# Kernel tuning notes

Measured on AMD Instinct MI355X. Metric: run time of the kernel, lower is better.

Reference implementation:

```python
import jax, jax.numpy as jnp
import numpy as np

NH = 4
TEMP = 0.5

def _ln(x, w, b):
    mu = x.mean(-1, keepdims=True)
    var = ((x - mu) ** 2).mean(-1, keepdims=True)
    return (x - mu) / jnp.sqrt(var + 1e-5) * w + b

def _encoder(x, bias, key_pad, layers):
    # pre-LN torch TransformerEncoder, relu FFN, dropout=0
    Wqkv, bqkv, Wo, bo, ln1w, ln1b, ln2w, ln2b, W1, b1, W2, b2 = layers
    B, L, H = x.shape
    d = H // NH
    scale = 1.0 / np.sqrt(d)
    for i in range(Wqkv.shape[0]):
        y = _ln(x, ln1w[i], ln1b[i])
        qkv = y @ Wqkv[i].T + bqkv[i]
        q, k, v = jnp.split(qkv, 3, axis=-1)
        q = q.reshape(B, L, NH, d).transpose(0, 2, 1, 3)
        k = k.reshape(B, L, NH, d).transpose(0, 2, 1, 3)
        v = v.reshape(B, L, NH, d).transpose(0, 2, 1, 3)
        s = jnp.einsum('bhqd,bhkd->bhqk', q, k) * scale
        if bias is not None:
            s = s + bias
        s = s + key_pad[:, None, None, :]
        a = jax.nn.softmax(s, axis=-1)
        o = jnp.einsum('bhqk,bhkd->bhqd', a, v).transpose(0, 2, 1, 3).reshape(B, L, H)
        x = x + o @ Wo[i].T + bo[i]
        y = _ln(x, ln2w[i], ln2b[i])
        x = x + jax.nn.relu(y @ W1[i].T + b1[i]) @ W2[i].T + b2[i]
    return x

def _layer_params(key, nl, H, F, sc=0.05):
    ks = jax.random.split(key, 4)
    return (jax.random.normal(ks[0], (nl, 3 * H, H)) * sc, jnp.zeros((nl, 3 * H)),
            jax.random.normal(ks[1], (nl, H, H)) * sc, jnp.zeros((nl, H)),
            jnp.ones((nl, H)), jnp.zeros((nl, H)), jnp.ones((nl, H)), jnp.zeros((nl, H)),
            jax.random.normal(ks[2], (nl, F, H)) * sc, jnp.zeros((nl, F)),
            jax.random.normal(ks[3], (nl, H, F)) * sc, jnp.zeros((nl, H)))

def setup_inputs():
    key = jax.random.key(0)
    IN, H, ED, F = 64, 128, 16, 256
    G, NPG = 8, 512
    N = G * NPG
    m, k = 4, 16
    T = N
    S = T * m
    EPS = 24
    E_loc = S * EPS
    E = 65536
    ks = jax.random.split(key, 13)
    x = jax.random.normal(ks[0], (N, IN))
    log_probs = -jnp.abs(jax.random.normal(ks[1], (S,)))
    root = jnp.repeat(jnp.arange(T), m)
    base = (root // NPG) * NPG
    rest = base[:, None] + jax.random.randint(ks[2], (S, k - 1), 0, NPG)
    nodes_sampled = jnp.concatenate([root[:, None], rest], axis=1)
    valid = jnp.ones((S * k,), dtype=bool)
    edge_index_sampled = jax.random.randint(ks[3], (2, E_loc), 0, k)
    edge_ptr = jnp.arange(S + 1) * EPS
    ea_flat = jax.random.normal(ks[4], (E_loc, ED))
    src = jax.random.randint(ks[5], (E,), 0, N)
    dst = (src // NPG) * NPG + jax.random.randint(ks[6], (E,), 0, NPG)
    edge_index = jnp.stack([src, dst])
    edge_attr = jax.random.normal(ks[7], (E, ED))
    batch_vec = jnp.arange(N) // NPG
    ptr = jnp.arange(G + 1) * NPG
    d = dict(x=x, log_probs=log_probs, ea_flat=ea_flat, edge_attr=edge_attr,
             init_W=jax.random.normal(ks[8], (H, IN + 2)) * 0.05, init_b=jnp.zeros((H,)),
             loc_ep_W=jax.random.normal(ks[9], (NH, ED)) * 0.05, loc_ep_b=jnp.zeros((NH,)),
             glob_ep_W=jax.random.normal(ks[10], (NH, ED)) * 0.05, glob_ep_b=jnp.zeros((NH,)),
             loc_nw=jnp.ones((H,)), loc_nb=jnp.zeros((H,)),
             glob_nw=jnp.ones((H,)), glob_nb=jnp.zeros((H,)),
             nodes_sampled=nodes_sampled, edge_index_sampled=edge_index_sampled,
             edge_ptr=edge_ptr, edge_index=edge_index, batch_vec=batch_vec,
             ptr=ptr, valid=valid)
    names = ['Wqkv', 'bqkv', 'Wo', 'bo', 'ln1w', 'ln1b', 'ln2w', 'ln2b', 'W1', 'b1', 'W2', 'b2']
    for n, a in zip(names, _layer_params(ks[11], 4, H, F)):
        d['loc_' + n] = a
    for n, a in zip(names, _layer_params(ks[12], 4, H, F)):
        d['glob_' + n] = a
    return d

def reference(x, log_probs, ea_flat, edge_attr, init_W, init_b, loc_ep_W, loc_ep_b,
              glob_ep_W, glob_ep_b, loc_nw, loc_nb, glob_nw, glob_nb,
              loc_Wqkv, loc_bqkv, loc_Wo, loc_bo, loc_ln1w, loc_ln1b, loc_ln2w, loc_ln2b,
              loc_W1, loc_b1, loc_W2, loc_b2,
              glob_Wqkv, glob_bqkv, glob_Wo, glob_bo, glob_ln1w, glob_ln1b, glob_ln2w, glob_ln2b,
              glob_W1, glob_b1, glob_W2, glob_b2,
              nodes_sampled, edge_index_sampled, edge_ptr, edge_index, batch_vec, ptr, valid):
    S, k = nodes_sampled.shape
    N = x.shape[0]
    T = N
    m = S // T
    G = ptr.shape[0] - 1
    max_N = N // G  # equal-size graphs
    H = init_W.shape[0]
    # ---- phase 1: flatten subgraphs + init features ----
    x_flat = x[nodes_sampled.reshape(-1)]                         # [S*k, IN]
    root_global = jnp.repeat(jnp.arange(T), m)                    # [S]
    root_local = jnp.argmax(nodes_sampled == root_global[:, None], axis=1)
    root_mask = jnp.zeros((S * k,), x.dtype).at[jnp.arange(S) * k + root_local].set(1.0)
    lp = jnp.where(jnp.isfinite(log_probs), log_probs, 0.0)
    lp_flat = jnp.repeat(lp, k)[:, None] * valid[:, None].astype(x.dtype)
    h = jnp.concatenate([x_flat, lp_flat, root_mask[:, None]], axis=1) @ init_W.T + init_b
    # ---- local edge bias (scatter-add) ----
    E_loc = ea_flat.shape[0]
    sub = jnp.searchsorted(edge_ptr, jnp.arange(E_loc), side='right') - 1
    eap = ea_flat @ loc_ep_W.T + loc_ep_b                         # [E_loc, NH]
    lbias = jnp.zeros((S, k, k, NH), x.dtype).at[sub, edge_index_sampled[0], edge_index_sampled[1]].add(eap).transpose(0, 3, 1, 2)
    v2 = valid.reshape(S, k)
    key_pad_l = jnp.where(v2, 0.0, -1e9).astype(x.dtype)
    loc_layers = (loc_Wqkv, loc_bqkv, loc_Wo, loc_bo, loc_ln1w, loc_ln1b, loc_ln2w, loc_ln2b, loc_W1, loc_b1, loc_W2, loc_b2)
    out = _encoder(h.reshape(S, k, H), lbias, key_pad_l, loc_layers)
    out = _ln(out, loc_nw, loc_nb)
    vf = v2.astype(x.dtype)[..., None]
    sub_embs = (out * vf).sum(1) / jnp.maximum(vf.sum(1), 1.0)    # [S, H]
    # ---- weighted-mean aggregation over m samples per target node ----
    w = jax.nn.softmax(log_probs.reshape(T, m) / TEMP, axis=1)
    node_embs = jnp.einsum('tm,tmh->th', w, sub_embs.reshape(T, m, H))
    # ---- global phase: to_dense_batch + edge-bias transformer ----
    pos = jnp.arange(N) - ptr[batch_vec]
    dense = jnp.zeros((G, max_N, H), x.dtype).at[batch_vec, pos].set(node_embs)
    vmask = jnp.zeros((G, max_N), bool).at[batch_vec, pos].set(True)
    g = batch_vec[edge_index[0]]
    sl = edge_index[0] - ptr[g]
    dl = edge_index[1] - ptr[g]
    eag = edge_attr @ glob_ep_W.T + glob_ep_b
    gbias = jnp.zeros((G, max_N, max_N, NH), x.dtype).at[g, sl, dl].add(eag).transpose(0, 3, 1, 2)
    key_pad_g = jnp.where(vmask, 0.0, -1e9).astype(x.dtype)
    glob_layers = (glob_Wqkv, glob_bqkv, glob_Wo, glob_bo, glob_ln1w, glob_ln1b, glob_ln2w, glob_ln2b, glob_W1, glob_b1, glob_W2, glob_b2)
    gout = _encoder(dense, gbias, key_pad_g, glob_layers)
    gout = _ln(gout, glob_nw, glob_nb)
    return (gout * vmask[..., None].astype(x.dtype)).sum(1)      # [G, H]
```

## Files before the change

### kernel.cpp

```cpp
#include <hip/hip_runtime.h>
#include <math.h>

#define IN_F      64
#define H_DIM     128
#define NH_       4
#define DH_       32
#define FF_DIM    256
#define KSUB      16
#define S_SEQ     16384
#define E_LOC     393216
#define G_NUM     8
#define NPG_      512
#define N_NODES   4096
#define E_GLOB    65536
#define NLAYERS   4
#define SCALE_ATT 0.17677669529663687f

#define WQKV_SZ   (3*H_DIM*H_DIM)
#define WO_SZ     (H_DIM*H_DIM)
#define W1_SZ     (FF_DIM*H_DIM)
#define W2_SZ     (H_DIM*FF_DIM)

#define ATT(sg)   (4352 + (sg) * 2560)
#define PS_OFF    9472
#define STG_SZ    10112

typedef __bf16 bf16x8 __attribute__((ext_vector_type(8)));
typedef float  f32x4  __attribute__((ext_vector_type(4)));

__device__ __forceinline__ unsigned short f2bf(float f) {
    unsigned u = __float_as_uint(f);
    unsigned r = (u + 0x7fffu + ((u >> 16) & 1u)) >> 16;
    return (unsigned short)r;
}

__device__ __forceinline__ unsigned cvt_pk(float lo, float hi) {
    unsigned r;
    asm("v_cvt_pk_bf16_f32 %0, %1, %2" : "=v"(r) : "v"(lo), "v"(hi));
    return r;
}

__device__ __forceinline__ f32x4 mfma16(bf16x8 a, bf16x8 b, f32x4 c) {
    return __builtin_amdgcn_mfma_f32_16x16x32_bf16(a, b, c, 0, 0, 0);
}

__device__ __forceinline__ void ln_to_row(const float (&X)[8][4],
    const float* __restrict__ w, const float* __restrict__ b,
    unsigned short* rowb, int r, int q)
{
    float s1[4] = {0,0,0,0}, s2[4] = {0,0,0,0};
    #pragma unroll
    for (int t = 0; t < 8; ++t)
        #pragma unroll
        for (int i = 0; i < 4; ++i) { float v = X[t][i]; s1[i] += v; s2[i] += v*v; }
    #pragma unroll
    for (int i = 0; i < 4; ++i) {
        float a = s1[i], c = s2[i];
        a += __shfl_xor(a, 1, 16); a += __shfl_xor(a, 2, 16);
        a += __shfl_xor(a, 4, 16); a += __shfl_xor(a, 8, 16);
        c += __shfl_xor(c, 1, 16); c += __shfl_xor(c, 2, 16);
        c += __shfl_xor(c, 4, 16); c += __shfl_xor(c, 8, 16);
        float mu = a * (1.f / H_DIM);
        float var = c * (1.f / H_DIM) - mu * mu;
        s1[i] = mu; s2[i] = rsqrtf(fmaxf(var, 0.f) + 1e-5f);
    }
    for (int t = 0; t < 8; ++t) {
        float wv = w[t * 16 + r], bv = b[t * 16 + r];
        float v0 = (X[t][0] - s1[0]) * s2[0] * wv + bv;
        float v1 = (X[t][1] - s1[1]) * s2[1] * wv + bv;
        float v2 = (X[t][2] - s1[2]) * s2[2] * wv + bv;
        float v3 = (X[t][3] - s1[3]) * s2[3] * wv + bv;
        unsigned lo = cvt_pk(v0, v1), hi = cvt_pk(v2, v3);
        rowb[(q * 4 + 0) * 136 + t * 16 + r] = (unsigned short)lo;
        rowb[(q * 4 + 1) * 136 + t * 16 + r] = (unsigned short)(lo >> 16);
        rowb[(q * 4 + 2) * 136 + t * 16 + r] = (unsigned short)hi;
        rowb[(q * 4 + 3) * 136 + t * 16 + r] = (unsigned short)(hi >> 16);
    }
}

__device__ __forceinline__ void ln_mean_out(const float (&X)[8][4],
    const float* __restrict__ fnw, const float* __restrict__ fnb,
    float* __restrict__ dst, int r, int q)
{
    float s1[4] = {0,0,0,0}, s2[4] = {0,0,0,0};
    #pragma unroll
    for (int t = 0; t < 8; ++t)
        #pragma unroll
        for (int i = 0; i < 4; ++i) { float v = X[t][i]; s1[i] += v; s2[i] += v*v; }
    #pragma unroll
    for (int i = 0; i < 4; ++i) {
        float a = s1[i], c = s2[i];
        a += __shfl_xor(a, 1, 16); a += __shfl_xor(a, 2, 16);
        a += __shfl_xor(a, 4, 16); a += __shfl_xor(a, 8, 16);
        c += __shfl_xor(c, 1, 16); c += __shfl_xor(c, 2, 16);
        c += __shfl_xor(c, 4, 16); c += __shfl_xor(c, 8, 16);
        float mu = a * (1.f / H_DIM);
        float var = c * (1.f / H_DIM) - mu * mu;
        s1[i] = mu; s2[i] = rsqrtf(fmaxf(var, 0.f) + 1e-5f);
    }
    float colsum[8];
    #pragma unroll
    for (int t = 0; t < 8; ++t) {
        float wv = fnw[t * 16 + r], bv = fnb[t * 16 + r];
        float cs = 0.f;
        #pragma unroll
        for (int i = 0; i < 4; ++i) cs += (X[t][i] - s1[i]) * s2[i] * wv + bv;
        cs += __shfl_xor(cs, 16, 64);
        cs += __shfl_xor(cs, 32, 64);
        colsum[t] = cs;
    }
    float c0 = (q == 0) ? colsum[0] : (q == 1) ? colsum[1] : (q == 2) ? colsum[2] : colsum[3];
    float c1 = (q == 0) ? colsum[4] : (q == 1) ? colsum[5] : (q == 2) ? colsum[6] : colsum[7];
    dst[q * 16 + r]       = c0 * (1.f / KSUB);
    dst[(q + 4) * 16 + r] = c1 * (1.f / KSUB);
}

__global__ __launch_bounds__(256) void conv_all_k(
    const float* __restrict__ lWqkv, const float* __restrict__ lWo,
    const float* __restrict__ lW1, const float* __restrict__ lW2,
    const float* __restrict__ x,
    const float* __restrict__ gWqkv, const float* __restrict__ gWo,
    const float* __restrict__ gW1, const float* __restrict__ gW2,
    const float* __restrict__ init_W,
    unsigned short* __restrict__ wq_b, unsigned short* __restrict__ wo_b,
    unsigned short* __restrict__ w1_b, unsigned short* __restrict__ w2_b,
    unsigned short* __restrict__ x_b,
    unsigned short* __restrict__ gwq_b, unsigned short* __restrict__ gwo_b,
    unsigned short* __restrict__ gw1_b, unsigned short* __restrict__ gw2_b,
    unsigned short* __restrict__ wi_b)
{
    int b = blockIdx.x, t = threadIdx.x;
    const float* src; unsigned short* dst; int base;
    if (b < 768)       { src = lWqkv; dst = wq_b;  base = b; }
    else if (b < 1024) { src = lWo;   dst = wo_b;  base = b - 768; }
    else if (b < 1536) { src = lW1;   dst = w1_b;  base = b - 1024; }
    else if (b < 2048) { src = lW2;   dst = w2_b;  base = b - 1536; }
    else if (b < 3072) { src = x;     dst = x_b;   base = b - 2048; }
    else if (b < 3840) { src = gWqkv; dst = gwq_b; base = b - 3072; }
    else if (b < 4096) { src = gWo;   dst = gwo_b; base = b - 3840; }
    else if (b < 4608) { src = gW1;   dst = gw1_b; base = b - 4096; }
    else if (b < 5120) { src = gW2;   dst = gw2_b; base = b - 4608; }
    else {
        int i = (b - 5120) * 256 + t;
        int row = i >> 6, c = i & 63;
        wi_b[i] = f2bf(init_W[row * 66 + c]);
        return;
    }
    int i = base * 256 + t;
    dst[i] = f2bf(src[i]);
}

__global__ __launch_bounds__(64) void local_encoder_k(
    const unsigned short* __restrict__ xb16,
    const float* __restrict__ log_probs,
    const float* __restrict__ ea_flat,
    const float* __restrict__ init_W,
    const float* __restrict__ init_b,
    const unsigned short* __restrict__ wi_b,
    const float* __restrict__ ep_W, const float* __restrict__ ep_b,
    const int* __restrict__ nodes, const int* __restrict__ eis,
    const unsigned short* __restrict__ wqb, const unsigned short* __restrict__ wob,
    const unsigned short* __restrict__ w1b, const unsigned short* __restrict__ w2b,
    const float* __restrict__ bqkv, const float* __restrict__ bo,
    const float* __restrict__ ln1w, const float* __restrict__ ln1b,
    const float* __restrict__ ln2w, const float* __restrict__ ln2b,
    const float* __restrict__ b1, const float* __restrict__ b2,
    const float* __restrict__ fnw, const float* __restrict__ fnb,
    float* __restrict__ sub_embs)
{
    __shared__ unsigned short stg[STG_SZ];

    const int lane = threadIdx.x & 63;
    const int r = lane & 15, q = lane >> 4;
    const int s0 = blockIdx.x * 2;
    float* biasWrk = (float*)(stg + 4352);

    {
        float2 z2f; z2f.x = 0.f; z2f.y = 0.f;
        for (int i = lane; i < 1024; i += 64) ((float2*)biasWrk)[i] = z2f;
        uint4 z4; z4.x = 0; z4.y = 0; z4.z = 0; z4.w = 0;
        for (int i = lane; i < 80; i += 64) ((uint4*)(stg + PS_OFF))[i] = z4;
    }

    int ndA = nodes[s0 * KSUB + r];
    int ndB = nodes[(s0 + 1) * KSUB + r];
    int rootA = s0 >> 2, rootB = (s0 + 1) >> 2;
    unsigned long long balA = __ballot((q == 0) && (ndA == rootA));
    unsigned long long balB = __ballot((q == 0) && (ndB == rootB));
    int rjA = balA ? (__ffsll((long long)balA) - 1) : 0;
    int rjB = balB ? (__ffsll((long long)balB) - 1) : 0;
    float lpA = log_probs[s0];     if (!isfinite(lpA)) lpA = 0.f;
    float lpB = log_probs[s0 + 1]; if (!isfinite(lpB)) lpB = 0.f;

    if (lane < 48) {
        int ls = lane / 24, ee = lane % 24;
        int e = (s0 + ls) * 24 + ee;
        int i0 = eis[e], i1 = eis[E_LOC + e];
        const float* ea = ea_flat + (size_t)e * 16;
        float4 e0 = *(const float4*)(ea), e1 = *(const float4*)(ea + 4);
        float4 e2 = *(const float4*)(ea + 8), e3 = *(const float4*)(ea + 12);
        #pragma unroll
        for (int h = 0; h < NH_; ++h) {
            const float* wp = ep_W + h * 16;
            float v = ep_b[h]
                + e0.x * wp[0]  + e0.y * wp[1]  + e0.z * wp[2]  + e0.w * wp[3]
                + e1.x * wp[4]  + e1.y * wp[5]  + e1.z * wp[6]  + e1.w * wp[7]
                + e2.x * wp[8]  + e2.y * wp[9]  + e2.z * wp[10] + e2.w * wp[11]
                + e3.x * wp[12] + e3.y * wp[13] + e3.z * wp[14] + e3.w * wp[15];
            atomicAdd(&biasWrk[ls * 1024 + (h * 16 + i0) * 16 + i1], v);
        }
    }

    for (int i2 = lane; i2 < 256; i2 += 64) {
        int sg = i2 >> 7, row = (i2 >> 3) & 15, seg = i2 & 7;
        int nd = __shfl(sg ? ndB : ndA, row, 64);
        *(uint4*)(stg + sg * 2176 + row * 136 + seg * 8) =
            *(const uint4*)(xb16 + (size_t)nd * IN_F + seg * 8);
    }

    float bT[2][NH_][4];
    #pragma unroll
    for (int sg = 0; sg < 2; ++sg)
        #pragma unroll
        for (int h = 0; h < NH_; ++h)
            #pragma unroll
            for (int i = 0; i < 4; ++i)
                bT[sg][h][i] = biasWrk[sg * 1024 + (h * 16 + q * 4 + i) * 16 + r];

    {
        uint2 z2; z2.x = 0; z2.y = 0;
        for (int i = lane; i < 320; i += 64) ((uint2*)(stg + ATT(0) + 1280))[i] = z2;
        for (int i = lane; i < 320; i += 64) ((uint2*)(stg + ATT(1) + 1280))[i] = z2;
    }

    float X[2][8][4];
    {
        bf16x8 aA0 = *(const bf16x8*)(stg + r * 136 + q * 8);
        bf16x8 aA1 = *(const bf16x8*)(stg + r * 136 + 32 + q * 8);
        bf16x8 aB0 = *(const bf16x8*)(stg + 2176 + r * 136 + q * 8);
        bf16x8 aB1 = *(const bf16x8*)(stg + 2176 + r * 136 + 32 + q * 8);
        const unsigned short* wr0 = wi_b + (size_t)r * 64 + q * 8;
        bf16x8 c0 = *(const bf16x8*)(wr0);
        bf16x8 c1 = *(const bf16x8*)(wr0 + 32);
        for (int t = 0; t < 8; ++t) {
            bf16x8 n0, n1;
            if (t < 7) {
                const unsigned short* wn = wr0 + (t + 1) * 1024;
                n0 = *(const bf16x8*)(wn);
                n1 = *(const bf16x8*)(wn + 32);
            }
            f32x4 accA = {0.f,0.f,0.f,0.f}, accB = {0.f,0.f,0.f,0.f};
            accA = mfma16(aA0, c0, accA); accA = mfma16(aA1, c1, accA);
            accB = mfma16(aB0, c0, accB); accB = mfma16(aB1, c1, accB);
            int o = t * 16 + r;
            float w64 = init_W[o * 66 + 64], w65 = init_W[o * 66 + 65], bb = init_b[o];
            #pragma unroll
            for (int i = 0; i < 4; ++i) {
                float vA = accA[i] + lpA * w64 + bb;
                float vB = accB[i] + lpB * w64 + bb;
                if (q * 4 + i == rjA) vA += w65;
                if (q * 4 + i == rjB) vB += w65;
                X[0][t][i] = vA; X[1][t][i] = vB;
            }
            c0 = n0; c1 = n1;
        }
    }

    for (int l = 0; l < NLAYERS; ++l) {
        const unsigned short* wq_l = wqb + (size_t)l * WQKV_SZ;
        const unsigned short* wo_l = wob + (size_t)l * WO_SZ;
        const unsigned short* w1_l = w1b + (size_t)l * W1_SZ;
        const unsigned short* w2_l = w2b + (size_t)l * W2_SZ;

        ln_to_row(X[0], ln1w + l * H_DIM, ln1b + l * H_DIM, stg, r, q);
        ln_to_row(X[1], ln1w + l * H_DIM, ln1b + l * H_DIM, stg + 2176, r, q);
        bf16x8 af[2][4];
        #pragma unroll
        for (int sg = 0; sg < 2; ++sg)
            #pragma unroll
            for (int kt = 0; kt < 4; ++kt)
                af[sg][kt] = *(const bf16x8*)(stg + sg * 2176 + r * 136 + kt * 32 + q * 8);

        for (int h = 0; h < NH_; ++h) {
            #pragma unroll
            for (int t = 0; t < 2; ++t) {
                #pragma unroll
                for (int p = 0; p < 3; ++p) {
                    const unsigned short* wr =
                        wq_l + (size_t)(p * H_DIM + h * DH_ + t * 16 + r) * H_DIM + q * 8;
                    bf16x8 c0 = *(const bf16x8*)(wr);
                    bf16x8 c1 = *(const bf16x8*)(wr + 32);
                    bf16x8 c2 = *(const bf16x8*)(wr + 64);
                    bf16x8 c3 = *(const bf16x8*)(wr + 96);
                    f32x4 aA = {0.f,0.f,0.f,0.f}, aB = {0.f,0.f,0.f,0.f};
                    aA = mfma16(af[0][0], c0, aA); aB = mfma16(af[1][0], c0, aB);
                    aA = mfma16(af[0][1], c1, aA); aB = mfma16(af[1][1], c1, aB);
                    aA = mfma16(af[0][2], c2, aA); aB = mfma16(af[1][2], c2, aB);
                    aA = mfma16(af[0][3], c3, aA); aB = mfma16(af[1][3], c3, aB);
                    float bb = bqkv[l * 384 + p * H_DIM + h * DH_ + t * 16 + r];
                    if (p < 2) {
                        int off = p * 640;
                        unsigned la = cvt_pk(aA[0] + bb, aA[1] + bb);
                        unsigned ha = cvt_pk(aA[2] + bb, aA[3] + bb);
                        unsigned lb = cvt_pk(aB[0] + bb, aB[1] + bb);
                        unsigned hb = cvt_pk(aB[2] + bb, aB[3] + bb);
                        stg[ATT(0) + off + (q * 4 + 0) * 40 + t * 16 + r] = (unsigned short)la;
                        stg[ATT(0) + off + (q * 4 + 1) * 40 + t * 16 + r] = (unsigned short)(la >> 16);
                        stg[ATT(0) + off + (q * 4 + 2) * 40 + t * 16 + r] = (unsigned short)ha;
                        stg[ATT(0) + off + (q * 4 + 3) * 40 + t * 16 + r] = (unsigned short)(ha >> 16);
                        stg[ATT(1) + off + (q * 4 + 0) * 40 + t * 16 + r] = (unsigned short)lb;
                        stg[ATT(1) + off + (q * 4 + 1) * 40 + t * 16 + r] = (unsigned short)(lb >> 16);
                        stg[ATT(1) + off + (q * 4 + 2) * 40 + t * 16 + r] = (unsigned short)hb;
                        stg[ATT(1) + off + (q * 4 + 3) * 40 + t * 16 + r] = (unsigned short)(hb >> 16);
                    } else {
                        uint2 pkA, pkB;
                        pkA.x = cvt_pk(aA[0] + bb, aA[1] + bb);
                        pkA.y = cvt_pk(aA[2] + bb, aA[3] + bb);
                        pkB.x = cvt_pk(aB[0] + bb, aB[1] + bb);
                        pkB.y = cvt_pk(aB[2] + bb, aB[3] + bb);
                        *(uint2*)(stg + ATT(0) + 1280 + (t * 16 + r) * 40 + q * 4) = pkA;
                        *(uint2*)(stg + ATT(1) + 1280 + (t * 16 + r) * 40 + q * 4) = pkB;
                    }
                }
            }
            #pragma unroll
            for (int sg = 0; sg < 2; ++sg) {
                const int ab = ATT(sg);
                bf16x8 aq = *(const bf16x8*)(stg + ab + r * 40 + q * 8);
                bf16x8 bk = *(const bf16x8*)(stg + ab + 640 + r * 40 + q * 8);
                f32x4 sc = mfma16(aq, bk, (f32x4){0.f,0.f,0.f,0.f});
                float pvv[4];
                #pragma unroll
                for (int i = 0; i < 4; ++i) {
                    float e = __expf(sc[i] * SCALE_ATT + bT[sg][h][i]);
                    float sum = e;
                    sum += __shfl_xor(sum, 1, 16); sum += __shfl_xor(sum, 2, 16);
                    sum += __shfl_xor(sum, 4, 16); sum += __shfl_xor(sum, 8, 16);
                    pvv[i] = e / sum;
                }
                unsigned plo = cvt_pk(pvv[0], pvv[1]);
                unsigned phi = cvt_pk(pvv[2], pvv[3]);
                stg[PS_OFF + (q * 4 + 0) * 40 + r] = (unsigned short)plo;
                stg[PS_OFF + (q * 4 + 1) * 40 + r] = (unsigned short)(plo >> 16);
                stg[PS_OFF + (q * 4 + 2) * 40 + r] = (unsigned short)phi;
                stg[PS_OFF + (q * 4 + 3) * 40 + r] = (unsigned short)(phi >> 16);
                bf16x8 ap = *(const bf16x8*)(stg + PS_OFF + r * 40 + q * 8);
                #pragma unroll
                for (int t = 0; t < 2; ++t) {
                    bf16x8 bv = *(const bf16x8*)(stg + ab + 1280 + (t * 16 + r) * 40 + q * 8);
                    f32x4 o = mfma16(ap, bv, (f32x4){0.f,0.f,0.f,0.f});
                    unsigned olo = cvt_pk(o[0], o[1]);
                    unsigned ohi = cvt_pk(o[2], o[3]);
                    stg[sg * 2176 + (q * 4 + 0) * 136 + h * DH_ + t * 16 + r] = (unsigned short)olo;
                    stg[sg * 2176 + (q * 4 + 1) * 136 + h * DH_ + t * 16 + r] = (unsigned short)(olo >> 16);
                    stg[sg * 2176 + (q * 4 + 2) * 136 + h * DH_ + t * 16 + r] = (unsigned short)ohi;
                    stg[sg * 2176 + (q * 4 + 3) * 136 + h * DH_ + t * 16 + r] = (unsigned short)(ohi >> 16);
                }
            }
        }

        {
            bf16x8 ao[2][4];
            #pragma unroll
            for (int sg = 0; sg < 2; ++sg)
                #pragma unroll
                for (int kt = 0; kt < 4; ++kt)
                    ao[sg][kt] = *(const bf16x8*)(stg + sg * 2176 + r * 136 + kt * 32 + q * 8);
            const unsigned short* wr0 = wo_l + (size_t)r * H_DIM + q * 8;
            bf16x8 co[4], no[4];
            #pragma unroll
            for (int kt = 0; kt < 4; ++kt) co[kt] = *(const bf16x8*)(wr0 + kt * 32);
            for (int nt = 0; nt < 8; ++nt) {
                if (nt < 7) {
                    const unsigned short* wn = wr0 + (size_t)(nt + 1) * 2048;
                    #pragma unroll
                    for (int kt = 0; kt < 4; ++kt) no[kt] = *(const bf16x8*)(wn + kt * 32);
                }
                f32x4 aA = {0.f,0.f,0.f,0.f}, aB = {0.f,0.f,0.f,0.f};
                #pragma unroll
                for (int kt = 0; kt < 4; ++kt) {
                    aA = mfma16(ao[0][kt], co[kt], aA);
                    aB = mfma16(ao[1][kt], co[kt], aB);
                }
                float bov = bo[l * H_DIM + nt * 16 + r];
                #pragma unroll
                for (int i = 0; i < 4; ++i) {
                    X[0][nt][i] += aA[i] + bov;
                    X[1][nt][i] += aB[i] + bov;
                }
                #pragma unroll
                for (int kt = 0; kt < 4; ++kt) co[kt] = no[kt];
            }
        }

        ln_to_row(X[0], ln2w + l * H_DIM, ln2b + l * H_DIM, stg, r, q);
        ln_to_row(X[1], ln2w + l * H_DIM, ln2b + l * H_DIM, stg + 2176, r, q);

        {
            bf16x8 a2[2][4];
            #pragma unroll
            for (int sg = 0; sg < 2; ++sg)
                #pragma unroll
                for (int kt = 0; kt < 4; ++kt)
                    a2[sg][kt] = *(const bf16x8*)(stg + sg * 2176 + r * 136 + kt * 32 + q * 8);
            const unsigned short* wr0 = w1_l + (size_t)r * H_DIM + q * 8;
            bf16x8 c1b[4], n1b[4];
            #pragma unroll
            for (int kt = 0; kt < 4; ++kt) c1b[kt] = *(const bf16x8*)(wr0 + kt * 32);
            for (int nt = 0; nt < 16; ++nt) {
                if (nt < 15) {
                    const unsigned short* wn = wr0 + (size_t)(nt + 1) * 2048;
                    #pragma unroll
                    for (int kt = 0; kt < 4; ++kt) n1b[kt] = *(const bf16x8*)(wn + kt * 32);
                }
                float b1v = b1[l * FF_DIM + nt * 16 + r];
                #pragma unroll
                for (int sg = 0; sg < 2; ++sg) {
                    f32x4 acc = {0.f,0.f,0.f,0.f};
                    #pragma unroll
                    for (int kt = 0; kt < 4; ++kt) acc = mfma16(a2[sg][kt], c1b[kt], acc);
                    float f0 = fmaxf(acc[0] + b1v, 0.f), f1 = fmaxf(acc[1] + b1v, 0.f);
                    float f2 = fmaxf(acc[2] + b1v, 0.f), f3 = fmaxf(acc[3] + b1v, 0.f);
                    unsigned flo = cvt_pk(f0, f1), fhi = cvt_pk(f2, f3);
                    stg[sg * 4224 + (q * 4 + 0) * 264 + nt * 16 + r] = (unsigned short)flo;
                    stg[sg * 4224 + (q * 4 + 1) * 264 + nt * 16 + r] = (unsigned short)(flo >> 16);
                    stg[sg * 4224 + (q * 4 + 2) * 264 + nt * 16 + r] = (unsigned short)fhi;
                    stg[sg * 4224 + (q * 4 + 3) * 264 + nt * 16 + r] = (unsigned short)(fhi >> 16);
                }
                #pragma unroll
                for (int kt = 0; kt < 4; ++kt) c1b[kt] = n1b[kt];
            }
            for (int kp = 0; kp < 2; ++kp) {
                bf16x8 a1[2][4];
                #pragma unroll
                for (int sg = 0; sg < 2; ++sg)
                    #pragma unroll
                    for (int kt = 0; kt < 4; ++kt)
                        a1[sg][kt] = *(const bf16x8*)(stg + sg * 4224 + r * 264 + kp * 128 + kt * 32 + q * 8);
                const unsigned short* wr2 = w2_l + (size_t)r * FF_DIM + kp * 128 + q * 8;
                bf16x8 c2b[4], n2b[4];
                #pragma unroll
                for (int kt = 0; kt < 4; ++kt) c2b[kt] = *(const bf16x8*)(wr2 + kt * 32);
                for (int nt = 0; nt < 8; ++nt) {
                    if (nt < 7) {
                        const unsigned short* wn = wr2 + (size_t)(nt + 1) * 4096;
                        #pragma unroll
                        for (int kt = 0; kt < 4; ++kt) n2b[kt] = *(const bf16x8*)(wn + kt * 32);
                    }
                    f32x4 aA = {0.f,0.f,0.f,0.f}, aB = {0.f,0.f,0.f,0.f};
                    #pragma unroll
                    for (int kt = 0; kt < 4; ++kt) {
                        aA = mfma16(a1[0][kt], c2b[kt], aA);
                        aB = mfma16(a1[1][kt], c2b[kt], aB);
                    }
                    float b2v = (kp == 0) ? b2[l * H_DIM + nt * 16 + r] : 0.f;
                    #pragma unroll
                    for (int i = 0; i < 4; ++i) {
                        X[0][nt][i] += aA[i] + b2v;
                        X[1][nt][i] += aB[i] + b2v;
                    }
                    #pragma unroll
                    for (int kt = 0; kt < 4; ++kt) c2b[kt] = n2b[kt];
                }
            }
        }
    }

    ln_mean_out(X[0], fnw, fnb, sub_embs + (size_t)s0 * H_DIM, r, q);
    ln_mean_out(X[1], fnw, fnb, sub_embs + (size_t)(s0 + 1) * H_DIM, r, q);
}

__global__ __launch_bounds__(256) void agg_ln_k(const float* __restrict__ sub,
    const float* __restrict__ lp, const int* __restrict__ bvec,
    const int* __restrict__ ptrg, const float* __restrict__ w,
    const float* __restrict__ b, float* __restrict__ xg,
    unsigned short* __restrict__ yout)
{
    int t = blockIdx.x * 16 + (threadIdx.x >> 4);
    int ln = threadIdx.x & 15;
    float l0 = lp[t * 4 + 0] * 2.f, l1 = lp[t * 4 + 1] * 2.f;
    float l2 = lp[t * 4 + 2] * 2.f, l3 = lp[t * 4 + 3] * 2.f;
    float mx = fmaxf(fmaxf(l0, l1), fmaxf(l2, l3));
    float e0 = __expf(l0 - mx), e1 = __expf(l1 - mx);
    float e2 = __expf(l2 - mx), e3 = __expf(l3 - mx);
    float inv = 1.f / (e0 + e1 + e2 + e3);
    e0 *= inv; e1 *= inv; e2 *= inv; e3 *= inv;
    int g = bvec[t];
    int row = g * NPG_ + (t - ptrg[g]);
    const float* sp = sub + (size_t)t * 4 * H_DIM;
    float v[8], s1 = 0.f, s2 = 0.f;
    #pragma unroll
    for (int k = 0; k < 8; ++k) {
        int i = ln + k * 16;
        float val = e0 * sp[i] + e1 * sp[H_DIM + i] + e2 * sp[2 * H_DIM + i]
                  + e3 * sp[3 * H_DIM + i];
        xg[(size_t)row * H_DIM + i] = val;
        v[k] = val; s1 += val; s2 += val * val;
    }
    for (int m2 = 8; m2 >= 1; m2 >>= 1) {
        s1 += __shfl_xor(s1, m2, 16);
        s2 += __shfl_xor(s2, m2, 16);
    }
    float mu = s1 * (1.f / H_DIM), var = s2 * (1.f / H_DIM) - mu * mu;
    float rs = rsqrtf(fmaxf(var, 0.f) + 1e-5f);
    #pragma unroll
    for (int k = 0; k < 8; ++k) {
        int i = ln + k * 16;
        yout[(size_t)row * H_DIM + i] = f2bf((v[k] - mu) * rs * w[i] + b[i]);
    }
}

__global__ __launch_bounds__(256) void zero_k(float4* __restrict__ p)
{
    p[(size_t)blockIdx.x * 256 + threadIdx.x] = make_float4(0.f, 0.f, 0.f, 0.f);
}

__global__ __launch_bounds__(256) void gbias_scatter_k(
    const float* __restrict__ edge_attr, const int* __restrict__ eidx,
    const int* __restrict__ bvec, const int* __restrict__ ptrg,
    const float* __restrict__ epW, const float* __restrict__ epb,
    float* __restrict__ gbias)
{
    int e = blockIdx.x * 256 + threadIdx.x;
    int src = eidx[e], dst = eidx[E_GLOB + e];
    int g = bvec[src];
    int sl = src - ptrg[g], dl = dst - ptrg[g];
    const float* ea = edge_attr + (size_t)e * 16;
    #pragma unroll
    for (int h = 0; h < NH_; ++h) {
        float v = epb[h];
        #pragma unroll
        for (int t = 0; t < 16; ++t) v += ea[t] * epW[h * 16 + t];
        atomicAdd(&gbias[(((size_t)g * NH_ + h) * NPG_ + sl) * NPG_ + dl], v);
    }
}

__global__ __launch_bounds__(256) void softmax_bf_k(float* __restrict__ sc)
{
    int row = blockIdx.x * 4 + (threadIdx.x >> 6);
    int lane = threadIdx.x & 63;
    float4* r4 = (float4*)(sc + (size_t)row * NPG_);
    float4 v0 = r4[lane * 2], v1 = r4[lane * 2 + 1];
    float mx = fmaxf(fmaxf(fmaxf(v0.x, v0.y), fmaxf(v0.z, v0.w)),
                     fmaxf(fmaxf(v1.x, v1.y), fmaxf(v1.z, v1.w)));
    for (int m2 = 32; m2 >= 1; m2 >>= 1) mx = fmaxf(mx, __shfl_xor(mx, m2, 64));
    v0.x = __expf(v0.x - mx); v0.y = __expf(v0.y - mx);
    v0.z = __expf(v0.z - mx); v0.w = __expf(v0.w - mx);
    v1.x = __expf(v1.x - mx); v1.y = __expf(v1.y - mx);
    v1.z = __expf(v1.z - mx); v1.w = __expf(v1.w - mx);
    float s = v0.x + v0.y + v0.z + v0.w + v1.x + v1.y + v1.z + v1.w;
    for (int m2 = 32; m2 >= 1; m2 >>= 1) s += __shfl_xor(s, m2, 64);
    float inv = 1.f / s;
    unsigned short p0 = f2bf(v0.x * inv), p1 = f2bf(v0.y * inv);
    unsigned short p2 = f2bf(v0.z * inv), p3 = f2bf(v0.w * inv);
    unsigned short p4 = f2bf(v1.x * inv), p5 = f2bf(v1.y * inv);
    unsigned short p6 = f2bf(v1.z * inv), p7 = f2bf(v1.w * inv);
    uint4 pk;
    pk.x = (unsigned)p0 | ((unsigned)p1 << 16);
    pk.y = (unsigned)p2 | ((unsigned)p3 << 16);
    pk.z = (unsigned)p4 | ((unsigned)p5 << 16);
    pk.w = (unsigned)p6 | ((unsigned)p7 << 16);
    *(uint4*)((unsigned short*)(sc + (size_t)row * NPG_) + lane * 8) = pk;
}

__global__ __launch_bounds__(256) void gemm_mfma_k(
    const unsigned short* __restrict__ A, const unsigned short* __restrict__ B,
    void* __restrict__ Cv, const float* __restrict__ bias, const float* __restrict__ D,
    unsigned short* __restrict__ vtout,
    int M, int N, int K, int lda, int ldb, int ldc, int ldd,
    long sAg, long sAh, long sBg, long sBh, long sCg, long sCh, long sDg, long sDh,
    float alpha, int op)
{
    const int z = blockIdx.z, zg = z >> 2, zh = z & 3;
    A += zg * sAg + zh * sAh;
    B += zg * sBg + zh * sBh;
    const int lane = threadIdx.x & 63, wave = threadIdx.x >> 6;
    const int r = lane & 15, q = lane >> 4;
    const int m0 = blockIdx.y * 64 + wave * 16;
    const int n0 = blockIdx.x * 64;
    const int ntiles = min(4, (N - n0) >> 4);
    const int KT = K >> 5;
    const unsigned short* ap = A + (size_t)(m0 + r) * lda + q * 8;
    for (int nt = 0; nt < ntiles; ++nt) {
        const int col = n0 + nt * 16 + r;
        const unsigned short* bp = B + (size_t)col * ldb + q * 8;
        f32x4 acc = {0.f, 0.f, 0.f, 0.f};
        for (int kc = 0; kc < KT; ++kc) {
            bf16x8 av = *(const bf16x8*)(ap + kc * 32);
            bf16x8 bv = *(const bf16x8*)(bp + kc * 32);
            acc = mfma16(av, bv, acc);
        }
        float bv2 = bias ? bias[col] : 0.f;
        #pragma unroll
        for (int i = 0; i < 4; ++i) {
            const int row = m0 + q * 4 + i;
            if (op == 0) {
                ((unsigned short*)Cv)[zg * sCg + zh * sCh + (size_t)row * ldc + col] =
                    f2bf(acc[i] + bv2);
            } else if (op == 1) {
                ((float*)Cv)[zg * sCg + zh * sCh + (size_t)row * ldc + col] =
                    alpha * acc[i] + (D ? D[zg * sDg + zh * sDh + (size_t)row * ldd + col] : 0.f);
            } else if (op == 2) {
                ((float*)Cv)[(size_t)row * ldc + col] += acc[i] + bv2;
            } else if (op == 3) {
                ((unsigned short*)Cv)[(size_t)row * ldc + col] = f2bf(fmaxf(acc[i] + bv2, 0.f));
            } else {
                unsigned short hv = f2bf(acc[i] + bv2);
                ((unsigned short*)Cv)[(size_t)row * ldc + col] = hv;
                if (col >= 256) {
                    int h = (col - 256) >> 5, d = (col - 256) & 31;
                    int g = row >> 9, tok = row & 511;
                    vtout[(((size_t)(g * 4 + h)) * 32 + d) * 512 + tok] = hv;
                }
            }
        }
    }
}

template <int KT>
__global__ __launch_bounds__(64) void gemm_ln_k(
    const unsigned short* __restrict__ A, const unsigned short* __restrict__ B,
    const float* __restrict__ bias, float* __restrict__ xg,
    const float* __restrict__ lnw, const float* __restrict__ lnb,
    void* __restrict__ yout, int mode)
{
    const int lane = threadIdx.x & 63;
    const int r = lane & 15, q = lane >> 4;
    const int m0 = blockIdx.x * 16;
    const int K = KT * 32;
    const unsigned short* ap = A + (size_t)(m0 + r) * K + q * 8;
    bf16x8 afr[KT];
    #pragma unroll
    for (int kc = 0; kc < KT; ++kc) afr[kc] = *(const bf16x8*)(ap + kc * 32);
    float v[8][4];
    #pragma unroll
    for (int nt = 0; nt < 8; ++nt) {
        const int col = nt * 16 + r;
        const unsigned short* bp = B + (size_t)col * K + q * 8;
        f32x4 acc = {0.f, 0.f, 0.f, 0.f};
        #pragma unroll
        for (int kc = 0; kc < KT; ++kc)
            acc = mfma16(afr[kc], *(const bf16x8*)(bp + kc * 32), acc);
        float bb = bias[col];
        #pragma unroll
        for (int i = 0; i < 4; ++i) {
            const int row = m0 + q * 4 + i;
            float nv = xg[(size_t)row * H_DIM + col] + acc[i] + bb;
            xg[(size_t)row * H_DIM + col] = nv;
            v[nt][i] = nv;
        }
    }
    float s1[4] = {0,0,0,0}, s2[4] = {0,0,0,0};
    #pragma unroll
    for (int nt = 0; nt < 8; ++nt)
        #pragma unroll
        for (int i = 0; i < 4; ++i) { float x = v[nt][i]; s1[i] += x; s2[i] += x * x; }
    #pragma unroll
    for (int i = 0; i < 4; ++i) {
        float a = s1[i], c = s2[i];
        a += __shfl_xor(a, 1, 16); a += __shfl_xor(a, 2, 16);
        a += __shfl_xor(a, 4, 16); a += __shfl_xor(a, 8, 16);
        c += __shfl_xor(c, 1, 16); c += __shfl_xor(c, 2, 16);
        c += __shfl_xor(c, 4, 16); c += __shfl_xor(c, 8, 16);
        float mu = a * (1.f / H_DIM);
        float var = c * (1.f / H_DIM) - mu * mu;
        s1[i] = mu; s2[i] = rsqrtf(fmaxf(var, 0.f) + 1e-5f);
    }
    #pragma unroll
    for (int nt = 0; nt < 8; ++nt) {
        const int col = nt * 16 + r;
        float wv = lnw[col], bv = lnb[col];
        #pragma unroll
        for (int i = 0; i < 4; ++i) {
            const int row = m0 + q * 4 + i;
            float ln = (v[nt][i] - s1[i]) * s2[i] * wv + bv;
            if (mode == 0) ((unsigned short*)yout)[(size_t)row * H_DIM + col] = f2bf(ln);
            else           ((float*)yout)[(size_t)row * H_DIM + col] = ln;
        }
    }
}

__global__ __launch_bounds__(128) void reduce_out_k(const float* __restrict__ yg,
                                                    float* __restrict__ out)
{
    int g = blockIdx.x, i = threadIdx.x;
    float s = 0.f;
    for (int t = 0; t < NPG_; ++t) s += yg[((size_t)(g * NPG_ + t)) * H_DIM + i];
    out[g * H_DIM + i] = s;
}

static inline void launch_gmm(hipStream_t st, const unsigned short* A, const unsigned short* B,
    void* C, const float* bias, const float* D, unsigned short* vt,
    int M, int N, int K, int lda, int ldb, int ldc, int ldd,
    long sAg, long sAh, long sBg, long sBh, long sCg, long sCh, long sDg, long sDh,
    float alpha, int op, int Z)
{
    dim3 grid((N + 63) / 64, M / 64, Z);
    hipLaunchKernelGGL(gemm_mfma_k, grid, dim3(256), 0, st, A, B, C, bias, D, vt,
        M, N, K, lda, ldb, ldc, ldd, sAg, sAh, sBg, sBh, sCg, sCh, sDg, sDh, alpha, op);
}

extern "C" void kernel_launch(void* const* d_in, const int* in_sizes, int n_in,
                              void* d_out, int out_size, void* d_ws, size_t ws_size,
                              hipStream_t stream)
{
    const float* x         = (const float*)d_in[0];
    const float* lp        = (const float*)d_in[1];
    const float* ea_flat   = (const float*)d_in[2];
    const float* edge_attr = (const float*)d_in[3];
    const float* init_W    = (const float*)d_in[4];
    const float* init_b    = (const float*)d_in[5];
    const float* lepW      = (const float*)d_in[6];
    const float* lepb      = (const float*)d_in[7];
    const float* gepW      = (const float*)d_in[8];
    const float* gepb      = (const float*)d_in[9];
    const float* lnw       = (const float*)d_in[10];
    const float* lnb       = (const float*)d_in[11];
    const float* gnw       = (const float*)d_in[12];
    const float* gnb       = (const float*)d_in[13];
    const int*   nodes     = (const int*)d_in[14];
    const int*   eis       = (const int*)d_in[15];
    const int*   eptr      = (const int*)d_in[16];  (void)eptr;
    const int*   eidx      = (const int*)d_in[17];
    const int*   bvec      = (const int*)d_in[18];
    const int*   ptrg      = (const int*)d_in[19];
    const float* lWqkv = (const float*)d_in[21];
    const float* lbqkv = (const float*)d_in[22];
    const float* lWo   = (const float*)d_in[23];
    const float* lbo   = (const float*)d_in[24];
    const float* lln1w = (const float*)d_in[25];
    const float* lln1b = (const float*)d_in[26];
    const float* lln2w = (const float*)d_in[27];
    const float* lln2b = (const float*)d_in[28];
    const float* lW1   = (const float*)d_in[29];
    const float* lb1   = (const float*)d_in[30];
    const float* lW2   = (const float*)d_in[31];
    const float* lb2   = (const float*)d_in[32];
    const float* gWqkv = (const float*)d_in[33];
    const float* gbqkv = (const float*)d_in[34];
    const float* gWo   = (const float*)d_in[35];
    const float* gbo   = (const float*)d_in[36];
    const float* gln1w = (const float*)d_in[37];
    const float* gln1b = (const float*)d_in[38];
    const float* gln2w = (const float*)d_in[39];
    const float* gln2b = (const float*)d_in[40];
    const float* gW1   = (const float*)d_in[41];
    const float* gb1   = (const float*)d_in[42];
    const float* gW2   = (const float*)d_in[43];
    const float* gb2   = (const float*)d_in[44];

    float* out = (float*)d_out;
    float* ws  = (float*)d_ws;
    float* gbias   = ws;
    float* scores  = ws + 8388608;
    float* subembs = scores;
    float* xg      = ws + 16777216;
    unsigned short* qkvg_b = (unsigned short*)(ws + 17301504);
    unsigned short* yg_b   = (unsigned short*)(ws + 18087936);
    unsigned short* attg_b = (unsigned short*)(ws + 18350080);
    unsigned short* ffg_b  = (unsigned short*)(ws + 18612224);
    unsigned short* vt_b   = (unsigned short*)(ws + 19136512);
    unsigned short* gw     = (unsigned short*)(ws + 19398656);

    unsigned short* wb   = (unsigned short*)gbias;
    unsigned short* wq_b = wb;
    unsigned short* wo_b = wb + 196608;
    unsigned short* w1_b = wb + 262144;
    unsigned short* w2_b = wb + 393216;
    unsigned short* x_b  = wb + 524288;
    unsigned short* wi_b = wb + 786432;
    unsigned short* gwq_b = gw;
    unsigned short* gwo_b = gw + 196608;
    unsigned short* gw1_b = gw + 262144;
    unsigned short* gw2_b = gw + 393216;

    hipLaunchKernelGGL(conv_all_k, dim3(5152), dim3(256), 0, stream,
        lWqkv, lWo, lW1, lW2, x, gWqkv, gWo, gW1, gW2, init_W,
        wq_b, wo_b, w1_b, w2_b, x_b, gwq_b, gwo_b, gw1_b, gw2_b, wi_b);

    hipLaunchKernelGGL(local_encoder_k, dim3(S_SEQ / 2), dim3(64), 0, stream,
        x_b, lp, ea_flat, init_W, init_b, wi_b, lepW, lepb, nodes, eis,
        wq_b, wo_b, w1_b, w2_b,
        lbqkv, lbo, lln1w, lln1b, lln2w, lln2b, lb1, lb2,
        lnw, lnb, subembs);

    hipLaunchKernelGGL(agg_ln_k, dim3(N_NODES / 16), dim3(256), 0, stream,
        subembs, lp, bvec, ptrg, gln1w, gln1b, xg, yg_b);

    hipLaunchKernelGGL(zero_k, dim3(8192), dim3(256), 0, stream, (float4*)gbias);
    hipLaunchKernelGGL(gbias_scatter_k, dim3(E_GLOB / 256), dim3(256), 0, stream,
        edge_attr, eidx, bvec, ptrg, gepW, gepb, gbias);

    for (int l = 0; l < NLAYERS; ++l) {
        launch_gmm(stream, yg_b, gwq_b + (size_t)l * WQKV_SZ, qkvg_b,
                   gbqkv + l * 384, nullptr, vt_b, 4096, 384, 128, 128, 128, 384, 0,
                   0, 0, 0, 0, 0, 0, 0, 0, 1.f, 4, 1);
        launch_gmm(stream, qkvg_b, qkvg_b + 128, scores, nullptr, gbias, nullptr,
                   512, 512, 32, 384, 384, 512, 512,
                   (long)512 * 384, 32, (long)512 * 384, 32,
                   1048576, 262144, 1048576, 262144, SCALE_ATT, 1, 32);
        hipLaunchKernelGGL(softmax_bf_k, dim3(4096), dim3(256), 0, stream, scores);
        launch_gmm(stream, (const unsigned short*)scores, vt_b, attg_b,
                   nullptr, nullptr, nullptr, 512, 32, 512, 1024, 512, 128, 0,
                   2097152, 524288, 65536, 16384, 65536, 32, 0, 0, 1.f, 0, 32);
        hipLaunchKernelGGL(gemm_ln_k<4>, dim3(256), dim3(64), 0, stream,
            attg_b, gwo_b + (size_t)l * WO_SZ, gbo + l * H_DIM, xg,
            gln2w + l * H_DIM, gln2b + l * H_DIM, (void*)yg_b, 0);
        launch_gmm(stream, yg_b, gw1_b + (size_t)l * W1_SZ, ffg_b,
                   gb1 + l * FF_DIM, nullptr, nullptr, 4096, 256, 128, 128, 128, 256, 0,
                   0, 0, 0, 0, 0, 0, 0, 0, 1.f, 3, 1);
        const float* nw = (l < 3) ? (gln1w + (l + 1) * H_DIM) : gnw;
        const float* nb = (l < 3) ? (gln1b + (l + 1) * H_DIM) : gnb;
        void* yo = (l < 3) ? (void*)yg_b : (void*)scores;
        hipLaunchKernelGGL(gemm_ln_k<8>, dim3(256), dim3(64), 0, stream,
            ffg_b, gw2_b + (size_t)l * W2_SZ, gb2 + l * H_DIM, xg,
            nw, nb, yo, (l < 3) ? 0 : 1);
    }

    hipLaunchKernelGGL(reduce_out_k, dim3(G_NUM), dim3(128), 0, stream, scores, out);
}
```

Baseline: 1.504 ms.

## Fuse global attention scores, softmax and PV into one kernel

Replaces the three-step global attention (QK^T GEMM writing fp32 scores with edge bias, a separate softmax pass, then a PV GEMM) with one fused kernel per 16-query tile. Each wave computes QK^T twice via MFMA (once for the row max, once for exp and sum), keeps unnormalized probabilities in LDS as bf16, and multiplies by V^T, normalizing at the end. This removes the round trip of the large fp32 score matrix through global memory and two launches per layer. In exchange it recomputes QK^T, reads gbias twice, and runs only 64-thread blocks, which may limit occupancy and latency hiding. An unused op==2 epilogue branch is also removed from the generic GEMM.

```diff
diff --git a/kernel.cpp b/kernel.cpp
--- a/kernel.cpp
+++ b/kernel.cpp
@@ -535,32 +535,81 @@
     }
 }
 
-__global__ __launch_bounds__(256) void softmax_bf_k(float* __restrict__ sc)
-{
-    int row = blockIdx.x * 4 + (threadIdx.x >> 6);
-    int lane = threadIdx.x & 63;
-    float4* r4 = (float4*)(sc + (size_t)row * NPG_);
-    float4 v0 = r4[lane * 2], v1 = r4[lane * 2 + 1];
-    float mx = fmaxf(fmaxf(fmaxf(v0.x, v0.y), fmaxf(v0.z, v0.w)),
-                     fmaxf(fmaxf(v1.x, v1.y), fmaxf(v1.z, v1.w)));
-    for (int m2 = 32; m2 >= 1; m2 >>= 1) mx = fmaxf(mx, __shfl_xor(mx, m2, 64));
-    v0.x = __expf(v0.x - mx); v0.y = __expf(v0.y - mx);
-    v0.z = __expf(v0.z - mx); v0.w = __expf(v0.w - mx);
-    v1.x = __expf(v1.x - mx); v1.y = __expf(v1.y - mx);
-    v1.z = __expf(v1.z - mx); v1.w = __expf(v1.w - mx);
-    float s = v0.x + v0.y + v0.z + v0.w + v1.x + v1.y + v1.z + v1.w;
-    for (int m2 = 32; m2 >= 1; m2 >>= 1) s += __shfl_xor(s, m2, 64);
-    float inv = 1.f / s;
-    unsigned short p0 = f2bf(v0.x * inv), p1 = f2bf(v0.y * inv);
-    unsigned short p2 = f2bf(v0.z * inv), p3 = f2bf(v0.w * inv);
-    unsigned short p4 = f2bf(v1.x * inv), p5 = f2bf(v1.y * inv);
-    unsigned short p6 = f2bf(v1.z * inv), p7 = f2bf(v1.w * inv);
-    uint4 pk;
-    pk.x = (unsigned)p0 | ((unsigned)p1 << 16);
-    pk.y = (unsigned)p2 | ((unsigned)p3 << 16);
-    pk.z = (unsigned)p4 | ((unsigned)p5 << 16);
-    pk.w = (unsigned)p6 | ((unsigned)p7 << 16);
-    *(uint4*)((unsigned short*)(sc + (size_t)row * NPG_) + lane * 8) = pk;
+__global__ __launch_bounds__(64) void attn_fused_k(
+    const unsigned short* __restrict__ qkv,
+    const unsigned short* __restrict__ vt,
+    const float* __restrict__ gbias,
+    unsigned short* __restrict__ attg)
+{
+    __shared__ unsigned short pbuf[16 * 522];
+    const int lane = threadIdx.x & 63;
+    const int r = lane & 15, q = lane >> 4;
+    const int qt = blockIdx.x, z = blockIdx.y;
+    const int g = z >> 2, h = z & 3;
+    const int qrow0 = qt * 16;
+
+    bf16x8 fq = *(const bf16x8*)(qkv + (size_t)(g * NPG_ + qrow0 + r) * 384
+                                 + h * DH_ + q * 8);
+    const float* gb = gbias + (size_t)z * NPG_ * NPG_ + (size_t)qrow0 * NPG_;
+    const unsigned short* kbase = qkv + (size_t)g * NPG_ * 384 + H_DIM + h * DH_ + q * 8;
+
+    float mx[4] = {-1e30f, -1e30f, -1e30f, -1e30f};
+    for (int kt = 0; kt < 32; ++kt) {
+        bf16x8 bk = *(const bf16x8*)(kbase + (size_t)(kt * 16 + r) * 384);
+        f32x4 sc = mfma16(fq, bk, (f32x4){0.f,0.f,0.f,0.f});
+        #pragma unroll
+        for (int i = 0; i < 4; ++i)
+            mx[i] = fmaxf(mx[i],
+                sc[i] * SCALE_ATT + gb[(size_t)(q * 4 + i) * NPG_ + kt * 16 + r]);
+    }
+    #pragma unroll
+    for (int i = 0; i < 4; ++i) {
+        mx[i] = fmaxf(mx[i], __shfl_xor(mx[i], 1, 16));
+        mx[i] = fmaxf(mx[i], __shfl_xor(mx[i], 2, 16));
+        mx[i] = fmaxf(mx[i], __shfl_xor(mx[i], 4, 16));
+        mx[i] = fmaxf(mx[i], __shfl_xor(mx[i], 8, 16));
+    }
+
+    float sm[4] = {0.f, 0.f, 0.f, 0.f};
+    for (int kt = 0; kt < 32; ++kt) {
+        bf16x8 bk = *(const bf16x8*)(kbase + (size_t)(kt * 16 + r) * 384);
+        f32x4 sc = mfma16(fq, bk, (f32x4){0.f,0.f,0.f,0.f});
+        float e0 = __expf(sc[0] * SCALE_ATT + gb[(size_t)(q * 4 + 0) * NPG_ + kt * 16 + r] - mx[0]);
+        float e1 = __expf(sc[1] * SCALE_ATT + gb[(size_t)(q * 4 + 1) * NPG_ + kt * 16 + r] - mx[1]);
+        float e2 = __expf(sc[2] * SCALE_ATT + gb[(size_t)(q * 4 + 2) * NPG_ + kt * 16 + r] - mx[2]);
+        float e3 = __expf(sc[3] * SCALE_ATT + gb[(size_t)(q * 4 + 3) * NPG_ + kt * 16 + r] - mx[3]);
+        sm[0] += e0; sm[1] += e1; sm[2] += e2; sm[3] += e3;
+        unsigned lo = cvt_pk(e0, e1), hi = cvt_pk(e2, e3);
+        pbuf[(q * 4 + 0) * 522 + kt * 16 + r] = (unsigned short)lo;
+        pbuf[(q * 4 + 1) * 522 + kt * 16 + r] = (unsigned short)(lo >> 16);
+        pbuf[(q * 4 + 2) * 522 + kt * 16 + r] = (unsigned short)hi;
+        pbuf[(q * 4 + 3) * 522 + kt * 16 + r] = (unsigned short)(hi >> 16);
+    }
+    float inv[4];
+    #pragma unroll
+    for (int i = 0; i < 4; ++i) {
+        float s = sm[i];
+        s += __shfl_xor(s, 1, 16); s += __shfl_xor(s, 2, 16);
+        s += __shfl_xor(s, 4, 16); s += __shfl_xor(s, 8, 16);
+        inv[i] = 1.f / s;
+    }
+
+    f32x4 oa = {0.f,0.f,0.f,0.f}, ob = {0.f,0.f,0.f,0.f};
+    const unsigned short* v0p = vt + (size_t)(z * 32 + r) * NPG_;
+    const unsigned short* v1p = vt + (size_t)(z * 32 + 16 + r) * NPG_;
+    for (int kc = 0; kc < 16; ++kc) {
+        bf16x8 ap  = *(const bf16x8*)(pbuf + r * 522 + kc * 32 + q * 8);
+        bf16x8 bv0 = *(const bf16x8*)(v0p + kc * 32 + q * 8);
+        bf16x8 bv1 = *(const bf16x8*)(v1p + kc * 32 + q * 8);
+        oa = mfma16(ap, bv0, oa);
+        ob = mfma16(ap, bv1, ob);
+    }
+    #pragma unroll
+    for (int i = 0; i < 4; ++i) {
+        size_t row = (size_t)(g * NPG_ + qrow0 + q * 4 + i) * H_DIM + h * DH_;
+        attg[row + r]      = f2bf(oa[i] * inv[i]);
+        attg[row + 16 + r] = f2bf(ob[i] * inv[i]);
+    }
 }
 
 __global__ __launch_bounds__(256) void gemm_mfma_k(
@@ -600,8 +649,6 @@
             } else if (op == 1) {
                 ((float*)Cv)[zg * sCg + zh * sCh + (size_t)row * ldc + col] =
                     alpha * acc[i] + (D ? D[zg * sDg + zh * sDh + (size_t)row * ldd + col] : 0.f);
-            } else if (op == 2) {
-                ((float*)Cv)[(size_t)row * ldc + col] += acc[i] + bv2;
             } else if (op == 3) {
                 ((unsigned short*)Cv)[(size_t)row * ldc + col] = f2bf(fmaxf(acc[i] + bv2, 0.f));
             } else {
@@ -795,14 +842,8 @@
         launch_gmm(stream, yg_b, gwq_b + (size_t)l * WQKV_SZ, qkvg_b,
                    gbqkv + l * 384, nullptr, vt_b, 4096, 384, 128, 128, 128, 384, 0,
                    0, 0, 0, 0, 0, 0, 0, 0, 1.f, 4, 1);
-        launch_gmm(stream, qkvg_b, qkvg_b + 128, scores, nullptr, gbias, nullptr,
-                   512, 512, 32, 384, 384, 512, 512,
-                   (long)512 * 384, 32, (long)512 * 384, 32,
-                   1048576, 262144, 1048576, 262144, SCALE_ATT, 1, 32);
-        hipLaunchKernelGGL(softmax_bf_k, dim3(4096), dim3(256), 0, stream, scores);
-        launch_gmm(stream, (const unsigned short*)scores, vt_b, attg_b,
-                   nullptr, nullptr, nullptr, 512, 32, 512, 1024, 512, 128, 0,
-                   2097152, 524288, 65536, 16384, 65536, 32, 0, 0, 1.f, 0, 32);
+        hipLaunchKernelGGL(attn_fused_k, dim3(NPG_ / 16, 32), dim3(64), 0, stream,
+            qkvg_b, vt_b, gbias, attg_b);
         hipLaunchKernelGGL(gemm_ln_k<4>, dim3(256), dim3(64), 0, stream,
             attg_b, gwo_b + (size_t)l * WO_SZ, gbo + l * H_DIM, xg,
             gln2w + l * H_DIM, gln2b + l * H_DIM, (void*)yg_b, 0);
```

Result: faster. 1.402 ms (-6.8%).
